# Kernel optimization log

Hardware: AMD Instinct MI355X
Metric: run time of the kernel (lower is better)

Reference implementation:

```python
import jax, jax.numpy as jnp
import numpy as np

N_NODES = 100000
N_EDGES = 3200000
D_IN = 128
D_OUT = 128


def setup_inputs() -> dict:
    key = jax.random.key(0)
    k1, k2, k3, k4 = jax.random.split(key, 4)
    x = jax.random.normal(k1, (N_NODES, D_IN), dtype=jnp.float32)
    W = jax.random.normal(k2, (D_OUT, D_IN), dtype=jnp.float32) * (1.0 / np.sqrt(D_IN))
    edge_weight = jax.random.uniform(k3, (N_EDGES,), dtype=jnp.float32)
    edge_index = jax.random.randint(k4, (2, N_EDGES), 0, N_NODES, dtype=jnp.int32)
    return {"x": x, "W": W, "edge_weight": edge_weight, "edge_index": edge_index}


def reference(x, W, edge_weight, edge_index):
    # spmm(flt, x): for each edge (r, c, w): agg[r] += w * x[c]
    rows = edge_index[0]
    cols = edge_index[1]
    msgs = edge_weight[:, None] * x[cols]                      # [E, D_IN]
    agg = jax.ops.segment_sum(msgs, rows, num_segments=x.shape[0])  # [N, D_IN]
    # nn.Linear(bias=False): agg @ W.T, then tanh activation
    return jnp.tanh(agg @ W.T)
```

## Files before the change

### kernel.cpp

```cpp
#include <hip/hip_runtime.h>
#include <hip/hip_fp16.h>
#include <cstdint>

#define NN 100000
#define NE 3200000
#define DD 128

#define NB 782
#define NBP 800
#define T3 6400
#define EPT 25

#define CAP 5120
#define RPT 20

typedef __attribute__((ext_vector_type(8))) short s8v;
typedef __attribute__((ext_vector_type(4))) float f4v;

__device__ __forceinline__ unsigned f2bf(float f) {
    unsigned u = __float_as_uint(f);
    return (u + 0x7fffu + ((u >> 16) & 1u)) >> 16;
}
__device__ __forceinline__ float bf2f(unsigned b) { return __uint_as_float(b << 16); }
__device__ __forceinline__ unsigned packhl(float v) {
    unsigned h = f2bf(v);
    unsigned l = f2bf(v - bf2f(h));
    return (h << 16) | l;
}
__device__ __forceinline__ float tanh_fast(float x) {
    float e = __expf(2.0f * x);
    return 1.0f - 2.0f / (e + 1.0f);
}
__device__ __forceinline__ int wswz(int o, int k) {
    int byte = (o << 8) + (k << 1);
    byte ^= (o & 7) << 4;
    return byte >> 1;
}

__global__ __launch_bounds__(256) void xcvt_k(
    const float* __restrict__ x, __half* __restrict__ xh)
{
    int i = (blockIdx.x * 256 + threadIdx.x) * 4;
    float4 v = *reinterpret_cast<const float4*>(x + i);
    __half2 a = __floats2half2_rn(v.x, v.y);
    __half2 b = __floats2half2_rn(v.z, v.w);
    uint2 o = { *reinterpret_cast<unsigned*>(&a), *reinterpret_cast<unsigned*>(&b) };
    *reinterpret_cast<uint2*>(xh + i) = o;
}

__global__ __launch_bounds__(256) void wcvt_k(
    const float* __restrict__ W, unsigned short* __restrict__ whl)
{
    int i = blockIdx.x * 256 + threadIdx.x;
    int o = i >> 7, k = i & 127;
    float f = W[i];
    unsigned h = f2bf(f);
    unsigned l = f2bf(f - bf2f(h));
    int idx = wswz(o, k);
    whl[idx]         = (unsigned short)h;
    whl[16384 + idx] = (unsigned short)l;
}

__global__ __launch_bounds__(256) void tile_scatter_k(
    const int* __restrict__ rows, const int* __restrict__ cols,
    const float* __restrict__ ew, int* __restrict__ bin_cursor,
    unsigned* __restrict__ b4, unsigned char* __restrict__ nloc)
{
    __shared__ int h[NBP];
    __shared__ int toff[NBP];
    __shared__ int pos[NBP];
    __shared__ int gb[NBP];
    __shared__ int ps[256];
    __shared__ unsigned rec4[T3];
    __shared__ unsigned char nl[T3];

    int t = threadIdx.x;
    int base = blockIdx.x * T3;

    for (int b = t; b < NBP; b += 256) h[b] = 0;
    __syncthreads();

    int rv[EPT];
    #pragma unroll
    for (int i = 0; i < EPT; ++i) {
        int e = base + i * 256 + t;
        rv[i] = rows[e];
        atomicAdd(&h[rv[i] >> 7], 1);
    }
    __syncthreads();

    int c[4]; int s0 = 0;
    #pragma unroll
    for (int j = 0; j < 4; ++j) {
        int b = 4 * t + j;
        c[j] = (b < NBP) ? h[b] : 0;
        s0 += c[j];
    }
    ps[t] = s0; __syncthreads();
    for (int off = 1; off < 256; off <<= 1) {
        int add = (t >= off) ? ps[t - off] : 0;
        __syncthreads();
        ps[t] += add;
        __syncthreads();
    }
    int excl = ps[t] - s0;
    #pragma unroll
    for (int j = 0; j < 4; ++j) {
        int b = 4 * t + j;
        if (b < NBP) { toff[b] = excl; pos[b] = excl; excl += c[j]; }
    }
    __syncthreads();

    for (int b = t; b < NB; b += 256)
        gb[b] = h[b] ? atomicAdd(&bin_cursor[b], h[b]) : 0;
    __syncthreads();

    #pragma unroll
    for (int i = 0; i < EPT; ++i) {
        int e = base + i * 256 + t;
        int r = rv[i];
        int b = r >> 7;
        int slot = atomicAdd(&pos[b], 1);
        float w = ew[e];
        int wfx = (int)(w * 32768.0f + 0.5f);
        if (wfx > 32767) wfx = 32767;
        rec4[slot] = (unsigned)cols[e] | ((unsigned)wfx << 17);
        nl[slot]   = (unsigned char)(r & 127);
    }
    __syncthreads();

    int wid = t >> 6, lane = t & 63;
    for (int chunk = wid; chunk < T3 / 64; chunk += 4) {
        int idx = chunk * 64 + lane;
        int lo = 0, hi = NB - 1;
        while (lo < hi) {
            int mid = (lo + hi + 1) >> 1;
            if (toff[mid] <= idx) lo = mid; else hi = mid - 1;
        }
        int rel = gb[lo] + (idx - toff[lo]);
        if (rel < CAP) {
            size_t d = (size_t)lo * CAP + rel;
            b4[d]   = rec4[idx];
            nloc[d] = nl[idx];
        }
    }
}

__global__ __launch_bounds__(256) void sort_bin_k(
    const int* __restrict__ bin_cursor,
    unsigned* __restrict__ b4, const unsigned char* __restrict__ nloc,
    int* __restrict__ node_off, int* __restrict__ node_cnt)
{
    __shared__ unsigned rec[CAP];
    __shared__ int lh[128], sc[128], lpos[128];

    int b = blockIdx.x, t = threadIdx.x;
    size_t start = (size_t)b * CAP;
    int cnt = bin_cursor[b];
    if (cnt > CAP) cnt = CAP;

    unsigned mr[RPT]; int mn[RPT];
    #pragma unroll
    for (int j = 0; j < RPT; ++j) {
        int idx = t + j * 256;
        mr[j] = (idx < cnt) ? b4[start + idx] : 0u;
        mn[j] = (idx < cnt) ? (int)nloc[start + idx] : 0;
    }

    if (t < 128) lh[t] = 0;
    __syncthreads();
    #pragma unroll
    for (int j = 0; j < RPT; ++j) {
        int idx = t + j * 256;
        if (idx < cnt) atomicAdd(&lh[mn[j]], 1);
    }
    __syncthreads();

    int v = (t < 128) ? lh[t] : 0;
    if (t < 128) sc[t] = v;
    __syncthreads();
    for (int off = 1; off < 128; off <<= 1) {
        int add = (t >= off && t < 128) ? sc[t - off] : 0;
        __syncthreads();
        if (t < 128) sc[t] += add;
        __syncthreads();
    }
    if (t < 128) {
        int excl = sc[t] - v;
        lpos[t] = excl;
        int node = b * 128 + t;
        if (node < NN) {
            node_off[node] = (int)start + excl;
            node_cnt[node] = v;
        }
    }
    __syncthreads();

    #pragma unroll
    for (int j = 0; j < RPT; ++j) {
        int idx = t + j * 256;
        if (idx < cnt) {
            int slot = atomicAdd(&lpos[mn[j]], 1);
            rec[slot] = mr[j];
        }
    }
    __syncthreads();

    for (int i = t; i < cnt; i += 256)
        b4[start + i] = rec[i];
}

__global__ __launch_bounds__(256) void gather_hf_k(
    const unsigned* __restrict__ xh,
    const unsigned* __restrict__ b4,
    const int* __restrict__ node_off, const int* __restrict__ node_cnt,
    unsigned* __restrict__ aggp)
{
    int node = blockIdx.x * 4 + (threadIdx.x >> 6);
    int lane = threadIdx.x & 63;
    int start = node_off[node];
    int end   = start + node_cnt[node];

    float2 acc = {0.f, 0.f};
    int i = start;
    for (; i + 7 < end; i += 8) {
        unsigned e[8]; unsigned v[8];
        #pragma unroll
        for (int j = 0; j < 8; ++j) e[j] = __builtin_nontemporal_load(b4 + i + j);
        #pragma unroll
        for (int j = 0; j < 8; ++j)
            v[j] = xh[(size_t)(e[j] & 0x1FFFFu) * 64 + lane];
        #pragma unroll
        for (int j = 0; j < 8; ++j) {
            float w = (float)(e[j] >> 17) * (1.0f / 32768.0f);
            __half2 h2 = *reinterpret_cast<__half2*>(&v[j]);
            float2 f2 = __half22float2(h2);
            acc.x += w * f2.x;
            acc.y += w * f2.y;
        }
    }
    for (; i < end; ++i) {
        unsigned e0 = b4[i];
        unsigned v0 = xh[(size_t)(e0 & 0x1FFFFu) * 64 + lane];
        float w = (float)(e0 >> 17) * (1.0f / 32768.0f);
        __half2 h2 = *reinterpret_cast<__half2*>(&v0);
        float2 f2 = __half22float2(h2);
        acc.x += w * f2.x;
        acc.y += w * f2.y;
    }

    uint2 o;
    o.x = packhl(acc.x);
    o.y = packhl(acc.y);
    reinterpret_cast<uint2*>(aggp + (size_t)node * DD)[lane] = o;
}

__device__ __forceinline__ void unpack8(uint4 a, uint4 b, s8v& hi, s8v& lo) {
    unsigned u[8] = {a.x, a.y, a.z, a.w, b.x, b.y, b.z, b.w};
    #pragma unroll
    for (int j = 0; j < 8; ++j) {
        hi[j] = (short)(u[j] >> 16);
        lo[j] = (short)(u[j] & 0xffffu);
    }
}

__global__ __launch_bounds__(256) void gemm_mfma_k(
    const unsigned* __restrict__ aggp, const unsigned short* __restrict__ whl,
    float* __restrict__ out)
{
    __shared__ __align__(16) unsigned short Wh[128 * 128];
    __shared__ __align__(16) unsigned short Wl[128 * 128];

    int t = threadIdx.x;
    {
        const uint4* src = reinterpret_cast<const uint4*>(whl);
        uint4* dh = reinterpret_cast<uint4*>(Wh);
        uint4* dl = reinterpret_cast<uint4*>(Wl);
        #pragma unroll
        for (int i = 0; i < 8; ++i) {
            dh[t + i * 256] = src[t + i * 256];
            dl[t + i * 256] = src[2048 + t + i * 256];
        }
    }
    __syncthreads();

    int lane = t & 63;
    int w    = t >> 6;
    int rbase = blockIdx.x * 128 + w * 32;
    int fr = lane & 15, fq = lane >> 4;

    f4v acc[2][8];
    #pragma unroll
    for (int rt = 0; rt < 2; ++rt)
        #pragma unroll
        for (int nt = 0; nt < 8; ++nt)
            acc[rt][nt] = 0.0f;

    #pragma unroll
    for (int ks = 0; ks < 4; ++ks) {
        int kb = ks * 32 + fq * 8;
        s8v ah[2], al[2];
        #pragma unroll
        for (int rt = 0; rt < 2; ++rt) {
            int r = rbase + rt * 16 + fr;
            int rc = (r < NN) ? r : (NN - 1);
            const uint4* p = reinterpret_cast<const uint4*>(aggp + (size_t)rc * DD + kb);
            unpack8(p[0], p[1], ah[rt], al[rt]);
        }
        #pragma unroll
        for (int nt = 0; nt < 8; ++nt) {
            int o = nt * 16 + fr;
            int kk = ks * 32 + fq * 8;
            s8v bh = *reinterpret_cast<const s8v*>(&Wh[wswz(o, kk)]);
            s8v bl = *reinterpret_cast<const s8v*>(&Wl[wswz(o, kk)]);
            #pragma unroll
            for (int rt = 0; rt < 2; ++rt) {
                acc[rt][nt] = __builtin_amdgcn_mfma_f32_16x16x32_bf16(ah[rt], bh, acc[rt][nt], 0, 0, 0);
                acc[rt][nt] = __builtin_amdgcn_mfma_f32_16x16x32_bf16(al[rt], bh, acc[rt][nt], 0, 0, 0);
                acc[rt][nt] = __builtin_amdgcn_mfma_f32_16x16x32_bf16(ah[rt], bl, acc[rt][nt], 0, 0, 0);
            }
        }
    }

    #pragma unroll
    for (int rt = 0; rt < 2; ++rt) {
        int rr = rbase + rt * 16 + fq * 4;
        #pragma unroll
        for (int nt = 0; nt < 8; ++nt) {
            int col = nt * 16 + fr;
            #pragma unroll
            for (int j = 0; j < 4; ++j) {
                int row = rr + j;
                if (row < NN)
                    out[(size_t)row * DD + col] = tanh_fast(acc[rt][nt][j]);
            }
        }
    }
}

__global__ __launch_bounds__(256) void scatter_k(
    const float* __restrict__ x, const float* __restrict__ ew,
    const int* __restrict__ rows, const int* __restrict__ cols,
    float* __restrict__ agg)
{
    int e    = blockIdx.x * 4 + (threadIdx.x >> 6);
    int lane = threadIdx.x & 63;
    int r = rows[e];
    int c = cols[e];
    float w = ew[e];
    float2 v = reinterpret_cast<const float2*>(x + (size_t)c * DD)[lane];
    float* ag = agg + (size_t)r * DD + lane * 2;
    atomicAdd(ag,     w * v.x);
    atomicAdd(ag + 1, w * v.y);
}

__global__ __launch_bounds__(256) void gemm_tanh_k(
    const float* __restrict__ agg, const float* __restrict__ W,
    float* __restrict__ out)
{
    __shared__ float Wt[DD][DD + 4];
    __shared__ float At[32][DD];

    int tid = threadIdx.x;
    for (int i = tid; i < DD * DD; i += 256) {
        int o = i >> 7, k = i & 127;
        Wt[k][o] = W[i];
    }
    int row0 = blockIdx.x * 32;
    for (int i = tid; i < 32 * DD; i += 256) {
        At[i >> 7][i & 127] = agg[(size_t)row0 * DD + i];
    }
    __syncthreads();

    int colg = tid & 31;
    int rowg = tid >> 5;
    int c0 = colg * 4;
    int r0 = rowg * 4;

    float acc[4][4] = {};
    for (int k = 0; k < DD; ++k) {
        float4 wv = *reinterpret_cast<const float4*>(&Wt[k][c0]);
        #pragma unroll
        for (int i = 0; i < 4; ++i) {
            float a = At[r0 + i][k];
            acc[i][0] += a * wv.x;
            acc[i][1] += a * wv.y;
            acc[i][2] += a * wv.z;
            acc[i][3] += a * wv.w;
        }
    }

    #pragma unroll
    for (int i = 0; i < 4; ++i) {
        int r = row0 + r0 + i;
        float4 o4 = { tanhf(acc[i][0]), tanhf(acc[i][1]),
                      tanhf(acc[i][2]), tanhf(acc[i][3]) };
        *reinterpret_cast<float4*>(&out[(size_t)r * DD + c0]) = o4;
    }
}

extern "C" void kernel_launch(void* const* d_in, const int* in_sizes, int n_in,
                              void* d_out, int out_size, void* d_ws, size_t ws_size,
                              hipStream_t stream) {
    const float* x  = (const float*)d_in[0];
    const float* W  = (const float*)d_in[1];
    const float* ew = (const float*)d_in[2];
    const int*   ei = (const int*)d_in[3];
    const int* rows = ei;
    const int* cols = ei + NE;
    float* out = (float*)d_out;
    unsigned* aggp = (unsigned*)d_out;

    size_t ints = (size_t)NB + (size_t)2 * NN;
    size_t hdr = (ints + 3) & ~(size_t)3;
    size_t nbucket = (size_t)NB * CAP;
    size_t need = hdr * 4 + nbucket * 4 + (size_t)NN * 64 * 4 + nbucket + 65536;

    if (ws_size >= need) {
        int* bin_cursor = (int*)d_ws;
        int* node_off   = bin_cursor + NB;
        int* node_cnt   = node_off + NN;
        unsigned* b4    = (unsigned*)((int*)d_ws + hdr);
        unsigned* xh    = b4 + nbucket;
        unsigned char* nloc = (unsigned char*)(xh + (size_t)NN * 64);
        unsigned short* whl = (unsigned short*)(nloc + nbucket);

        hipMemsetAsync(bin_cursor, 0, (size_t)NB * sizeof(int), stream);
        xcvt_k<<<NN * DD / 1024, 256, 0, stream>>>(x, (__half*)xh);
        wcvt_k<<<64, 256, 0, stream>>>(W, whl);
        tile_scatter_k<<<NE / T3, 256, 0, stream>>>(rows, cols, ew, bin_cursor, b4, nloc);
        sort_bin_k<<<NB, 256, 0, stream>>>(bin_cursor, b4, nloc, node_off, node_cnt);
        gather_hf_k<<<NN / 4, 256, 0, stream>>>(xh, b4, node_off, node_cnt, aggp);
        gemm_mfma_k<<<NB, 256, 0, stream>>>(aggp, whl, out);
    } else {
        hipMemsetAsync(out, 0, (size_t)NN * DD * sizeof(float), stream);
        scatter_k<<<NE / 4, 256, 0, stream>>>(x, ew, rows, cols, out);
        gemm_tanh_k<<<NN / 32, 256, 0, stream>>>(out, W, out);
    }
}
```

Measured before the change: 267.0 us.

## Fuse preprocessing kernels and merge bin sort with gather in shared memory

The x and W conversion kernels are folded into the edge binning kernel as extra block ranges, so three launches become one and they can run concurrently. The per-bin sort and the gather are fused: each 512-thread block sorts its bin's edges into LDS and then gathers neighbour features straight from the LDS records. This removes the write-back of sorted records and the node offset/count arrays to global memory. In exchange, gather parallelism drops from 25000 small blocks to 782 large blocks that each handle 128 nodes, which may hurt load balance and latency hiding.

```diff
diff --git a/kernel.cpp b/kernel.cpp
--- a/kernel.cpp
+++ b/kernel.cpp
@@ -12,7 +12,11 @@
 #define EPT 25
 
 #define CAP 5120
-#define RPT 20
+#define RPT2 10
+
+#define NSCAT 500
+#define NXC   12500
+#define NWC   64
 
 typedef __attribute__((ext_vector_type(8))) short s8v;
 typedef __attribute__((ext_vector_type(4))) float f4v;
@@ -37,34 +41,13 @@
     return byte >> 1;
 }
 
-__global__ __launch_bounds__(256) void xcvt_k(
-    const float* __restrict__ x, __half* __restrict__ xh)
-{
-    int i = (blockIdx.x * 256 + threadIdx.x) * 4;
-    float4 v = *reinterpret_cast<const float4*>(x + i);
-    __half2 a = __floats2half2_rn(v.x, v.y);
-    __half2 b = __floats2half2_rn(v.z, v.w);
-    uint2 o = { *reinterpret_cast<unsigned*>(&a), *reinterpret_cast<unsigned*>(&b) };
-    *reinterpret_cast<uint2*>(xh + i) = o;
-}
-
-__global__ __launch_bounds__(256) void wcvt_k(
-    const float* __restrict__ W, unsigned short* __restrict__ whl)
-{
-    int i = blockIdx.x * 256 + threadIdx.x;
-    int o = i >> 7, k = i & 127;
-    float f = W[i];
-    unsigned h = f2bf(f);
-    unsigned l = f2bf(f - bf2f(h));
-    int idx = wswz(o, k);
-    whl[idx]         = (unsigned short)h;
-    whl[16384 + idx] = (unsigned short)l;
-}
-
-__global__ __launch_bounds__(256) void tile_scatter_k(
+__global__ __launch_bounds__(256) void pre_k(
     const int* __restrict__ rows, const int* __restrict__ cols,
-    const float* __restrict__ ew, int* __restrict__ bin_cursor,
-    unsigned* __restrict__ b4, unsigned char* __restrict__ nloc)
+    const float* __restrict__ ew, const float* __restrict__ x,
+    const float* __restrict__ W,
+    int* __restrict__ bin_cursor,
+    unsigned* __restrict__ b4, unsigned char* __restrict__ nloc,
+    __half* __restrict__ xh, unsigned short* __restrict__ whl)
 {
     __shared__ int h[NBP];
     __shared__ int toff[NBP];
@@ -74,8 +57,32 @@
     __shared__ unsigned rec4[T3];
     __shared__ unsigned char nl[T3];
 
+    int B = blockIdx.x;
     int t = threadIdx.x;
-    int base = blockIdx.x * T3;
+
+    if (B >= NSCAT) {
+        if (B < NSCAT + NXC) {
+            int i = ((B - NSCAT) * 256 + t) * 4;
+            float4 v = *reinterpret_cast<const float4*>(x + i);
+            __half2 a = __floats2half2_rn(v.x, v.y);
+            __half2 b2 = __floats2half2_rn(v.z, v.w);
+            uint2 o = { *reinterpret_cast<unsigned*>(&a),
+                        *reinterpret_cast<unsigned*>(&b2) };
+            *reinterpret_cast<uint2*>(xh + i) = o;
+        } else {
+            int i = (B - NSCAT - NXC) * 256 + t;
+            int o = i >> 7, k = i & 127;
+            float f = W[i];
+            unsigned hh = f2bf(f);
+            unsigned ll = f2bf(f - bf2f(hh));
+            int idx = wswz(o, k);
+            whl[idx]         = (unsigned short)hh;
+            whl[16384 + idx] = (unsigned short)ll;
+        }
+        return;
+    }
+
+    int base = B * T3;
 
     for (int b = t; b < NBP; b += 256) h[b] = 0;
     __syncthreads();
@@ -146,23 +153,25 @@
     }
 }
 
-__global__ __launch_bounds__(256) void sort_bin_k(
+__global__ __launch_bounds__(512) void bin_gather_k(
+    const unsigned* __restrict__ xh,
     const int* __restrict__ bin_cursor,
-    unsigned* __restrict__ b4, const unsigned char* __restrict__ nloc,
-    int* __restrict__ node_off, int* __restrict__ node_cnt)
+    const unsigned* __restrict__ b4, const unsigned char* __restrict__ nloc,
+    unsigned* __restrict__ aggp)
 {
     __shared__ unsigned rec[CAP];
     __shared__ int lh[128], sc[128], lpos[128];
+    __shared__ int noff[128], ncnt[128];
 
     int b = blockIdx.x, t = threadIdx.x;
     size_t start = (size_t)b * CAP;
     int cnt = bin_cursor[b];
     if (cnt > CAP) cnt = CAP;
 
-    unsigned mr[RPT]; int mn[RPT];
-    #pragma unroll
-    for (int j = 0; j < RPT; ++j) {
-        int idx = t + j * 256;
+    unsigned mr[RPT2]; int mn[RPT2];
+    #pragma unroll
+    for (int j = 0; j < RPT2; ++j) {
+        int idx = t + j * 512;
         mr[j] = (idx < cnt) ? b4[start + idx] : 0u;
         mn[j] = (idx < cnt) ? (int)nloc[start + idx] : 0;
     }
@@ -170,8 +179,8 @@
     if (t < 128) lh[t] = 0;
     __syncthreads();
     #pragma unroll
-    for (int j = 0; j < RPT; ++j) {
-        int idx = t + j * 256;
+    for (int j = 0; j < RPT2; ++j) {
+        int idx = t + j * 512;
         if (idx < cnt) atomicAdd(&lh[mn[j]], 1);
     }
     __syncthreads();
@@ -188,17 +197,14 @@
     if (t < 128) {
         int excl = sc[t] - v;
         lpos[t] = excl;
-        int node = b * 128 + t;
-        if (node < NN) {
-            node_off[node] = (int)start + excl;
-            node_cnt[node] = v;
-        }
-    }
-    __syncthreads();
-
-    #pragma unroll
-    for (int j = 0; j < RPT; ++j) {
-        int idx = t + j * 256;
+        noff[t] = excl;
+        ncnt[t] = v;
+    }
+    __syncthreads();
+
+    #pragma unroll
+    for (int j = 0; j < RPT2; ++j) {
+        int idx = t + j * 512;
         if (idx < cnt) {
             int slot = atomicAdd(&lpos[mn[j]], 1);
             rec[slot] = mr[j];
@@ -206,53 +212,44 @@
     }
     __syncthreads();
 
-    for (int i = t; i < cnt; i += 256)
-        b4[start + i] = rec[i];
-}
-
-__global__ __launch_bounds__(256) void gather_hf_k(
-    const unsigned* __restrict__ xh,
-    const unsigned* __restrict__ b4,
-    const int* __restrict__ node_off, const int* __restrict__ node_cnt,
-    unsigned* __restrict__ aggp)
-{
-    int node = blockIdx.x * 4 + (threadIdx.x >> 6);
-    int lane = threadIdx.x & 63;
-    int start = node_off[node];
-    int end   = start + node_cnt[node];
-
-    float2 acc = {0.f, 0.f};
-    int i = start;
-    for (; i + 7 < end; i += 8) {
-        unsigned e[8]; unsigned v[8];
-        #pragma unroll
-        for (int j = 0; j < 8; ++j) e[j] = __builtin_nontemporal_load(b4 + i + j);
-        #pragma unroll
-        for (int j = 0; j < 8; ++j)
-            v[j] = xh[(size_t)(e[j] & 0x1FFFFu) * 64 + lane];
-        #pragma unroll
-        for (int j = 0; j < 8; ++j) {
-            float w = (float)(e[j] >> 17) * (1.0f / 32768.0f);
-            __half2 h2 = *reinterpret_cast<__half2*>(&v[j]);
+    int wid = t >> 6, lane = t & 63;
+    for (int ni = wid; ni < 128; ni += 8) {
+        int node = b * 128 + ni;
+        if (node >= NN) break;
+        int s1 = noff[ni];
+        int e1 = s1 + ncnt[ni];
+        float2 acc = {0.f, 0.f};
+        int i = s1;
+        for (; i + 7 < e1; i += 8) {
+            unsigned e[8]; unsigned v8[8];
+            #pragma unroll
+            for (int j = 0; j < 8; ++j) e[j] = rec[i + j];
+            #pragma unroll
+            for (int j = 0; j < 8; ++j)
+                v8[j] = xh[(size_t)(e[j] & 0x1FFFFu) * 64 + lane];
+            #pragma unroll
+            for (int j = 0; j < 8; ++j) {
+                float w = (float)(e[j] >> 17) * (1.0f / 32768.0f);
+                __half2 h2 = *reinterpret_cast<__half2*>(&v8[j]);
+                float2 f2 = __half22float2(h2);
+                acc.x += w * f2.x;
+                acc.y += w * f2.y;
+            }
+        }
+        for (; i < e1; ++i) {
+            unsigned er = rec[i];
+            unsigned v0 = xh[(size_t)(er & 0x1FFFFu) * 64 + lane];
+            float w = (float)(er >> 17) * (1.0f / 32768.0f);
+            __half2 h2 = *reinterpret_cast<__half2*>(&v0);
             float2 f2 = __half22float2(h2);
             acc.x += w * f2.x;
             acc.y += w * f2.y;
         }
-    }
-    for (; i < end; ++i) {
-        unsigned e0 = b4[i];
-        unsigned v0 = xh[(size_t)(e0 & 0x1FFFFu) * 64 + lane];
-        float w = (float)(e0 >> 17) * (1.0f / 32768.0f);
-        __half2 h2 = *reinterpret_cast<__half2*>(&v0);
-        float2 f2 = __half22float2(h2);
-        acc.x += w * f2.x;
-        acc.y += w * f2.y;
-    }
-
-    uint2 o;
-    o.x = packhl(acc.x);
-    o.y = packhl(acc.y);
-    reinterpret_cast<uint2*>(aggp + (size_t)node * DD)[lane] = o;
+        uint2 o;
+        o.x = packhl(acc.x);
+        o.y = packhl(acc.y);
+        reinterpret_cast<uint2*>(aggp + (size_t)node * DD)[lane] = o;
+    }
 }
 
 __device__ __forceinline__ void unpack8(uint4 a, uint4 b, s8v& hi, s8v& lo) {
@@ -411,26 +408,21 @@
     float* out = (float*)d_out;
     unsigned* aggp = (unsigned*)d_out;
 
-    size_t ints = (size_t)NB + (size_t)2 * NN;
-    size_t hdr = (ints + 3) & ~(size_t)3;
+    size_t hdr = ((size_t)NB + 3) & ~(size_t)3;
     size_t nbucket = (size_t)NB * CAP;
     size_t need = hdr * 4 + nbucket * 4 + (size_t)NN * 64 * 4 + nbucket + 65536;
 
     if (ws_size >= need) {
         int* bin_cursor = (int*)d_ws;
-        int* node_off   = bin_cursor + NB;
-        int* node_cnt   = node_off + NN;
         unsigned* b4    = (unsigned*)((int*)d_ws + hdr);
         unsigned* xh    = b4 + nbucket;
         unsigned char* nloc = (unsigned char*)(xh + (size_t)NN * 64);
         unsigned short* whl = (unsigned short*)(nloc + nbucket);
 
         hipMemsetAsync(bin_cursor, 0, (size_t)NB * sizeof(int), stream);
-        xcvt_k<<<NN * DD / 1024, 256, 0, stream>>>(x, (__half*)xh);
-        wcvt_k<<<64, 256, 0, stream>>>(W, whl);
-        tile_scatter_k<<<NE / T3, 256, 0, stream>>>(rows, cols, ew, bin_cursor, b4, nloc);
-        sort_bin_k<<<NB, 256, 0, stream>>>(bin_cursor, b4, nloc, node_off, node_cnt);
-        gather_hf_k<<<NN / 4, 256, 0, stream>>>(xh, b4, node_off, node_cnt, aggp);
+        pre_k<<<NSCAT + NXC + NWC, 256, 0, stream>>>(
+            rows, cols, ew, x, W, bin_cursor, b4, nloc, (__half*)xh, whl);
+        bin_gather_k<<<NB, 512, 0, stream>>>(xh, bin_cursor, b4, nloc, aggp);
         gemm_mfma_k<<<NB, 256, 0, stream>>>(aggp, whl, out);
     } else {
         hipMemsetAsync(out, 0, (size_t)NN * DD * sizeof(float), stream);
```

Result: faster. 259.3 us (-2.9%).
